# Kernel optimization log

Hardware: AMD Instinct MI355X
Metric: run time of the kernel (lower is better)

## Reference

```python
import jax, jax.numpy as jnp
import numpy as np
from jax import lax

V, D, H, HD, L, E, HID, TOPK, B, T = 32000, 1024, 16, 64, 2, 4, 2048, 2, 1, 1024
EPS = 1e-8


def setup_inputs() -> dict:
    key = jax.random.key(0)
    ks = jax.random.split(key, 10)
    s = 0.02
    so = 0.02 / np.sqrt(2 * L)  # o_proj / down_proj init std
    return dict(
        idx=jax.random.randint(ks[0], (B, T), 0, V),
        tok_emb=jax.random.normal(ks[1], (V, D), jnp.float32) * s,
        attn_norm_w=jnp.ones((L, D), jnp.float32),
        q_w=jax.random.normal(ks[2], (L, D, D), jnp.float32) * s,
        q_b=jnp.zeros((L, D), jnp.float32),
        kv_w=jax.random.normal(ks[3], (L, D, 2 * D), jnp.float32) * s,
        kv_b=jnp.zeros((L, 2 * D), jnp.float32),
        o_w=jax.random.normal(ks[4], (L, D, D), jnp.float32) * so,
        o_b=jnp.zeros((L, D), jnp.float32),
        ffn_norm_w=jnp.ones((L, D), jnp.float32),
        router_w=jax.random.normal(ks[5], (L, D, E), jnp.float32) * s,
        gate_w=jax.random.normal(ks[6], (L, E, D, HID), jnp.float32) * s,
        up_w=jax.random.normal(ks[7], (L, E, D, HID), jnp.float32) * s,
        down_w=jax.random.normal(ks[8], (L, E, HID, D), jnp.float32) * so,
        lnf_w=jnp.ones((D,), jnp.float32),
    )


def _rms(x, w):
    return x / jnp.sqrt(jnp.mean(x * x, axis=-1, keepdims=True) + EPS) * w


def reference(idx, tok_emb, attn_norm_w, q_w, q_b, kv_w, kv_b, o_w, o_b,
              ffn_norm_w, router_w, gate_w, up_w, down_w, lnf_w):
    x = tok_emb[idx]  # [B,T,D]

    # ALiBi bias and causal mask (built once; block_size == T here)
    slopes = jnp.arange(1, H + 1, dtype=jnp.float32) / H          # [H]
    pos = jnp.arange(T, dtype=jnp.float32)
    alibi = slopes[:, None, None] * (pos[None, None, :] - pos[None, :, None])  # [H,T,T]
    causal = jnp.arange(T)[None, :] > jnp.arange(T)[:, None]      # True above diagonal

    for l in range(L):
        # --- causal self-attention with ALiBi ---
        h = _rms(x, attn_norm_w[l])
        q = (h @ q_w[l] + q_b[l]).reshape(B, T, H, HD)
        kv = (h @ kv_w[l] + kv_b[l]).reshape(B, T, 2, H, HD)
        k, v = kv[:, :, 0], kv[:, :, 1]
        att = jnp.einsum('bqhd,bkhd->bhqk', q, k) * (1.0 / np.sqrt(HD))
        att = att + alibi[None]
        att = jnp.where(causal, -jnp.inf, att)
        a = jax.nn.softmax(att, axis=-1)
        y = jnp.einsum('bhqk,bkhd->bqhd', a, v).reshape(B, T, D)
        x = x + y @ o_w[l] + o_b[l]

        # --- MoE FFN (top-k routing, SwiGLU experts, depth-scaled down_proj) ---
        hm = _rms(x, ffn_norm_w[l]).reshape(B * T, D)             # [N,D]
        rlog = hm @ router_w[l]                                   # [N,E]
        vals, sel = lax.top_k(rlog, TOPK)                         # [N,K]
        w = jax.nn.softmax(vals.astype(jnp.float32), axis=-1).astype(hm.dtype)
        # dense per-expert compute, combined sparsely via routing weights
        g = jax.nn.silu(jnp.einsum('nd,edh->enh', hm, gate_w[l])) \
            * jnp.einsum('nd,edh->enh', hm, up_w[l])              # [E,N,HID]
        out_e = jnp.einsum('enh,ehd->end', g, down_w[l]) * (1.0 / np.sqrt(l + 1))
        combine = jnp.sum(jax.nn.one_hot(sel, E, dtype=hm.dtype) * w[..., None], axis=1)  # [N,E]
        moe = jnp.einsum('ne,end->nd', combine, out_e).reshape(B, T, D)
        x = x + moe

    logits = _rms(x, lnf_w) @ tok_emb.T  # tied head weight
    return logits
```

## Files before the change

kernel.cpp:

```cpp
#include <hip/hip_runtime.h>
#include <cmath>

typedef __attribute__((ext_vector_type(8))) _Float16 f16x8;
typedef __attribute__((ext_vector_type(8))) unsigned short u16x8;
typedef __attribute__((ext_vector_type(4))) float f32x4;

#define DEV static __device__ __forceinline__

constexpr int Dm   = 1024;
constexpr int HIDm = 2048;
constexpr int NT   = 1024;
constexpr int NV   = 32000;
constexpr float EPSf  = 1e-8f;
constexpr float LOSC  = 4096.0f;
constexpr float ILOSC = 1.0f / 4096.0f;

DEV unsigned short h2u(_Float16 h){ union{_Float16 h; unsigned short u;} v; v.h=h; return v.u; }

DEV f32x4 MF(f16x8 a, f16x8 b, f32x4 c){ return __builtin_amdgcn_mfma_f32_16x16x32_f16(a,b,c,0,0,0); }

typedef __attribute__((address_space(1))) void GV;
typedef __attribute__((address_space(3))) void LV;
DEV void gll16(const void* g, void* l){
  __builtin_amdgcn_global_load_lds((GV*)(__UINTPTR_TYPE__)g, (LV*)l, 16, 0, 0);
}

DEV int swk(int lane){ return (((lane&3) ^ ((lane>>3)&3))*8); }
DEV int rdc(int fr, int fg){ return ((fg ^ ((fr>>1)&3))*8); }

template<int SPLIT>
DEV void st_sp(unsigned short* __restrict__ hi, unsigned short* __restrict__ lo, size_t o, float v){
  _Float16 hh = (_Float16)v;
  hi[o] = h2u(hh);
  if constexpr (SPLIT==3) lo[o] = h2u((_Float16)((v - (float)hh)*LOSC));
}

__global__ __launch_bounds__(256) void k_gather(
    const int* __restrict__ idx, const float* __restrict__ emb, float* __restrict__ x)
{
  const int t = blockIdx.x;
  const int d = threadIdx.x*4;
  *(float4*)&x[(size_t)t*Dm + d] = *(const float4*)&emb[(size_t)idx[t]*Dm + d];
}

__global__ __launch_bounds__(256) void k_cvt16(
    const float* __restrict__ src, unsigned short* __restrict__ dst)
{
  const size_t i = ((size_t)blockIdx.x*256 + threadIdx.x)*8;
  const float4 v0 = *(const float4*)&src[i];
  const float4 v1 = *(const float4*)&src[i+4];
  u16x8 h;
  h[0]=h2u((_Float16)v0.x); h[1]=h2u((_Float16)v0.y);
  h[2]=h2u((_Float16)v0.z); h[3]=h2u((_Float16)v0.w);
  h[4]=h2u((_Float16)v1.x); h[5]=h2u((_Float16)v1.y);
  h[6]=h2u((_Float16)v1.z); h[7]=h2u((_Float16)v1.w);
  *(u16x8*)&dst[i] = h;
}

template<int SPLIT>
__global__ __launch_bounds__(256) void k_rms(
    const float* __restrict__ x, const float* __restrict__ w,
    unsigned short* __restrict__ ohi, unsigned short* __restrict__ olo)
{
  const int t = blockIdx.x, tid = threadIdx.x;
  const float* row = x + (size_t)t*Dm;
  float s = 0.f;
  #pragma unroll
  for (int i=0;i<4;++i){ const float v = row[tid + i*256]; s += v*v; }
  #pragma unroll
  for (int d=1; d<64; d<<=1) s += __shfl_xor(s, d);
  __shared__ float red[4];
  if ((tid&63)==0) red[tid>>6] = s;
  __syncthreads();
  const float tot = red[0]+red[1]+red[2]+red[3];
  const float rstd = rsqrtf(tot*(1.0f/Dm) + EPSf);
  #pragma unroll
  for (int i=0;i<4;++i){
    const int c = tid + i*256;
    st_sp<SPLIT>(ohi, olo, (size_t)t*Dm + c, row[c]*rstd*w[c]);
  }
}

__global__ __launch_bounds__(64) void k_router(
    const float* __restrict__ x, const float* __restrict__ nw,
    const float* __restrict__ rw, float* __restrict__ cmb)
{
  const int t = blockIdx.x, lane = threadIdx.x;
  const float* row = x + (size_t)t*Dm;
  float ss = 0.f;
  for (int i=lane; i<Dm; i+=64) ss += row[i]*row[i];
  #pragma unroll
  for (int d=1; d<64; d<<=1) ss += __shfl_xor(ss, d);
  const float rstd = rsqrtf(ss*(1.0f/Dm) + EPSf);
  float lg0=0,lg1=0,lg2=0,lg3=0;
  for (int i=lane; i<Dm; i+=64){
    const float hm = row[i]*rstd*nw[i];
    lg0 += hm*rw[i*4+0]; lg1 += hm*rw[i*4+1];
    lg2 += hm*rw[i*4+2]; lg3 += hm*rw[i*4+3];
  }
  #pragma unroll
  for (int d=1; d<64; d<<=1){
    lg0 += __shfl_xor(lg0,d); lg1 += __shfl_xor(lg1,d);
    lg2 += __shfl_xor(lg2,d); lg3 += __shfl_xor(lg3,d);
  }
  if (lane==0){
    float lg[4] = {lg0,lg1,lg2,lg3};
    int s0 = 0;
    for (int e=1;e<4;++e) if (lg[e] > lg[s0]) s0 = e;
    int s1 = -1;
    for (int e=0;e<4;++e){ if (e==s0) continue; if (s1<0 || lg[e] > lg[s1]) s1 = e; }
    const float eb2 = expf(lg[s1] - lg[s0]);
    const float inv = 1.0f/(1.0f + eb2);
    float o[4] = {0.f,0.f,0.f,0.f};
    o[s0] = inv; o[s1] = eb2*inv;
    cmb[t*4+0]=o[0]; cmb[t*4+1]=o[1]; cmb[t*4+2]=o[2]; cmb[t*4+3]=o[3];
  }
}

__global__ __launch_bounds__(256) void k_scan(
    const float* __restrict__ cmb, int* __restrict__ tl,
    float* __restrict__ cwl, int* __restrict__ cnt)
{
  const int e = threadIdx.x>>6, lane = threadIdx.x&63;
  int base = 0;
  for (int t0=0; t0<NT; t0+=64){
    const float w = cmb[(size_t)(t0+lane)*4 + e];
    const unsigned long long m = __ballot(w > 0.f);
    const int pre = __popcll(m & ((1ull<<lane)-1ull));
    if (w > 0.f){ tl[e*NT + base + pre] = t0+lane; cwl[e*NT + base + pre] = w; }
    base += __popcll(m);
  }
  if (lane==0) cnt[e] = base;
}

template<int SPLIT>
__global__ __launch_bounds__(256) void k_wconv(
    const float* __restrict__ W, unsigned short* __restrict__ Whi,
    unsigned short* __restrict__ Wlo, int K, int N)
{
  __shared__ float tile[64][65];
  const int t = threadIdx.x;
  const int n0 = blockIdx.x*64, k0 = blockIdx.y*64;
  const size_t eb = (size_t)blockIdx.z * (size_t)K * N;
  const int r = t>>2;
  #pragma unroll
  for (int i=0;i<4;++i){
    const int c = (t&3)*16 + i*4;
    *(float4*)&tile[r][c] = *(const float4*)&W[eb + (size_t)(k0+r)*N + n0 + c];
  }
  __syncthreads();
  const int n = t>>2;
  #pragma unroll
  for (int i=0;i<2;++i){
    const int kc = (t&3)*8 + i*32;
    u16x8 hi, lo;
    #pragma unroll
    for (int j=0;j<8;++j){
      const float v = tile[kc+j][n];
      const _Float16 hh = (_Float16)v;
      hi[j] = h2u(hh);
      if constexpr (SPLIT==3) lo[j] = h2u((_Float16)((v-(float)hh)*LOSC));
      else lo[j] = 0;
    }
    *(u16x8*)&Whi[eb + (size_t)(n0+n)*K + k0 + kc] = hi;
    if constexpr (SPLIT==3) *(u16x8*)&Wlo[eb + (size_t)(n0+n)*K + k0 + kc] = lo;
  }
}

template<int SPLIT, int ZMODE>
__global__ __launch_bounds__(256) void k_mm(
    const unsigned short* __restrict__ Ahi, const unsigned short* __restrict__ Alo,
    const unsigned short* __restrict__ Bhi, const unsigned short* __restrict__ Blo,
    float* __restrict__ part, int lda, int ldb, int K, int ldo)
{
  constexpr int PL = (SPLIT==3)?2:1;
  __shared__ __align__(16) unsigned short As[PL][128][32];
  __shared__ __align__(16) unsigned short Bs[PL][128][32];
  const int tid=threadIdx.x, wv=tid>>6, lane=tid&63, fr=lane&15, fg=lane>>4;
  const int n0=blockIdx.x*128, r0=blockIdx.y*128, zz=blockIdx.z;
  const int wr=(wv>>1)*64, wc=(wv&1)*64;
  const int sr=lane>>2, sk=swk(lane);
  const int rc = rdc(fr, fg);

  const f32x4 z4={0.f,0.f,0.f,0.f};
  f32x4 accM[4][4], accC[4][4];
  #pragma unroll
  for (int i=0;i<4;++i)
    #pragma unroll
    for (int j=0;j<4;++j){ accM[i][j]=z4; accC[i][j]=z4; }

  for (int kt=0; kt<K; kt+=32){
    #pragma unroll
    for (int i=0;i<2;++i){
      const int rr = wv*32 + i*16 + sr;
      size_t ao, bo;
      if constexpr (ZMODE==2){
        ao = (size_t)(r0+rr)*lda + zz*K + kt + sk;
        bo = (size_t)(n0+rr)*ldb + zz*K + kt + sk;
      } else {
// ... 13 lines not shown
      for (int p=0;p<PL;++p) a[rt][p] = *(const f16x8*)&As[p][wr+rt*16+fr][rc];
    #pragma unroll
    for (int ct=0;ct<4;++ct)
      #pragma unroll
      for (int p=0;p<PL;++p) b[ct][p] = *(const f16x8*)&Bs[p][wc+ct*16+fr][rc];
    #pragma unroll
    for (int rt=0;rt<4;++rt)
      #pragma unroll
      for (int ct=0;ct<4;++ct){
        accM[rt][ct] = MF(a[rt][0], b[ct][0], accM[rt][ct]);
        if constexpr (SPLIT==3){
          accC[rt][ct] = MF(a[rt][0], b[ct][1], accC[rt][ct]);
          accC[rt][ct] = MF(a[rt][1], b[ct][0], accC[rt][ct]);
        }
      }
    __syncthreads();
  }

  #pragma unroll
  for (int rt=0;rt<4;++rt)
    #pragma unroll
    for (int ct=0;ct<4;++ct)
      #pragma unroll
      for (int j=0;j<4;++j){
        const int row = r0 + wr + rt*16 + fg*4 + j;
        const int col = n0 + wc + ct*16 + fr;
        float v = accM[rt][ct][j];
        if constexpr (SPLIT==3) v += accC[rt][ct][j]*ILOSC;
        part[((size_t)zz*NT + row)*ldo + col] = v;
      }
}

template<int SPLIT>
__global__ __launch_bounds__(256) void k_comb_qk(
    const float* __restrict__ part, const float* __restrict__ qb, const float* __restrict__ kvb,
    unsigned short* __restrict__ qhi, unsigned short* __restrict__ qlo,
    unsigned short* __restrict__ khi, unsigned short* __restrict__ klo)
{
  const int t = blockIdx.x;
  #pragma unroll
  for (int i=0;i<2;++i){
    const int col = threadIdx.x*4 + i*1024;
    const float4 p0 = *(const float4*)&part[(size_t)t*3072 + col];
    const float4 p1 = *(const float4*)&part[((size_t)NT + t)*3072 + col];
    float v[4] = {p0.x+p1.x, p0.y+p1.y, p0.z+p1.z, p0.w+p1.w};
    #pragma unroll
    for (int j=0;j<4;++j){
      const int c = col + j;
      if (c < Dm) st_sp<SPLIT>(qhi, qlo, (size_t)t*Dm + c, v[j] + qb[c]);
      else        st_sp<SPLIT>(khi, klo, (size_t)t*Dm + (c-Dm), v[j] + kvb[c-Dm]);
    }
  }
}

template<int SPLIT>
__global__ __launch_bounds__(256) void k_combvT(
    const float* __restrict__ part, const float* __restrict__ kvb,
    unsigned short* __restrict__ vthi, unsigned short* __restrict__ vtlo)
{
  __shared__ float tile[64][65];
  const int d0 = blockIdx.x*64, t0 = blockIdx.y*64;
  const int tid = threadIdx.x;
  {
    const int tl_ = tid>>2, dc = (tid&3)*16;
    #pragma unroll
    for (int i=0;i<4;++i){
      const int d = dc + i*4;
      const float4 p0 = *(const float4*)&part[(size_t)(t0+tl_)*3072 + 2048 + d0 + d];
      const float4 p1 = *(const float4*)&part[((size_t)NT + t0+tl_)*3072 + 2048 + d0 + d];
      tile[tl_][d+0] = p0.x+p1.x + kvb[1024+d0+d+0];
      tile[tl_][d+1] = p0.y+p1.y + kvb[1024+d0+d+1];
      tile[tl_][d+2] = p0.z+p1.z + kvb[1024+d0+d+2];
      tile[tl_][d+3] = p0.w+p1.w + kvb[1024+d0+d+3];
    }
  }
  __syncthreads();
  #pragma unroll
  for (int i=0;i<2;++i){
    const int u = tid + i*256;
    const int dl = u>>3, tch = (u&7)*8;
    u16x8 hi, lo;
    #pragma unroll
    for (int j=0;j<8;++j){
      const float v = tile[tch+j][dl];
      const _Float16 hh = (_Float16)v;
      hi[j] = h2u(hh);
      if constexpr (SPLIT==3) lo[j] = h2u((_Float16)((v-(float)hh)*LOSC));
      else lo[j] = 0;
    }
    *(u16x8*)&vthi[(size_t)(d0+dl)*NT + t0 + tch] = hi;
    if constexpr (SPLIT==3) *(u16x8*)&vtlo[(size_t)(d0+dl)*NT + t0 + tch] = lo;
  }
}

template<int SPLIT>
__global__ __launch_bounds__(256) void k_down(
    const unsigned short* __restrict__ Ahi, const unsigned short* __restrict__ Alo,
    const unsigned short* __restrict__ Bhi, const unsigned short* __restrict__ Blo,
    const int* __restrict__ tl, const int* __restrict__ cnt,
    float* __restrict__ part)
{
  constexpr int PL = (SPLIT==3)?2:1;
  const int zz = blockIdx.z, e = zz>>1, ks = zz&1;
  const int r0 = blockIdx.y*128, n0 = blockIdx.x*128;
  const int cn = cnt[e];
  if (r0 >= cn) return;
  __shared__ __align__(16) unsigned short As[PL][128][32];
  __shared__ __align__(16) unsigned short Bs[PL][128][32];
  __shared__ int tl_s[128];
  const int tid=threadIdx.x, wv=tid>>6, lane=tid&63, fr=lane&15, fg=lane>>4;
  const int wr=(wv>>1)*64, wc=(wv&1)*64;
  const int sr=lane>>2, sk=swk(lane);
  const int rc = rdc(fr, fg);
  if (tid < 128) tl_s[tid] = (r0+tid < cn) ? tl[e*NT + r0 + tid] : -1;

  const f32x4 z4={0.f,0.f,0.f,0.f};
  f32x4 accM[4][4], accC[4][4];
  #pragma unroll
  for (int i=0;i<4;++i)
    #pragma unroll
    for (int j=0;j<4;++j){ accM[i][j]=z4; accC[i][j]=z4; }

  const int kbeg = ks*1024, kend = kbeg + 1024;
  for (int kt=kbeg; kt<kend; kt+=32){
// ... 13 lines not shown
    for (int rt=0;rt<4;++rt)
      #pragma unroll
      for (int p=0;p<PL;++p) a[rt][p] = *(const f16x8*)&As[p][wr+rt*16+fr][rc];
    #pragma unroll
    for (int ct=0;ct<4;++ct)
      #pragma unroll
      for (int p=0;p<PL;++p) b[ct][p] = *(const f16x8*)&Bs[p][wc+ct*16+fr][rc];
    #pragma unroll
    for (int rt=0;rt<4;++rt)
      #pragma unroll
      for (int ct=0;ct<4;++ct){
        accM[rt][ct] = MF(a[rt][0], b[ct][0], accM[rt][ct]);
        if constexpr (SPLIT==3){
          accC[rt][ct] = MF(a[rt][0], b[ct][1], accC[rt][ct]);
          accC[rt][ct] = MF(a[rt][1], b[ct][0], accC[rt][ct]);
        }
      }
    __syncthreads();
  }

  #pragma unroll
  for (int rt=0;rt<4;++rt)
    #pragma unroll
    for (int ct=0;ct<4;++ct)
      #pragma unroll
      for (int j=0;j<4;++j){
        const int i = wr + rt*16 + fg*4 + j;
        const int col = n0 + wc + ct*16 + fr;
        float v = accM[rt][ct][j];
        if constexpr (SPLIT==3) v += accC[rt][ct][j]*ILOSC;
        const int tok = tl_s[i];
        if (tok >= 0) part[((size_t)zz*NT + tok)*Dm + col] = v;
      }
}

template<int SK, bool BIAS>
__global__ __launch_bounds__(256) void k_comb(
    const float* __restrict__ part, const float* __restrict__ bias, float* __restrict__ x)
{
  const int row = blockIdx.x;
  const int c = threadIdx.x*4;
  float4 s = *(float4*)&x[(size_t)row*Dm + c];
  #pragma unroll
  for (int z=0; z<SK; ++z){
    const float4 p = *(const float4*)&part[((size_t)z*NT + row)*Dm + c];
    s.x+=p.x; s.y+=p.y; s.z+=p.z; s.w+=p.w;
  }
  if constexpr (BIAS){
    const float4 b = *(const float4*)&bias[c];
    s.x+=b.x; s.y+=b.y; s.z+=b.z; s.w+=b.w;
  }
  *(float4*)&x[(size_t)row*Dm + c] = s;
}

__global__ __launch_bounds__(256) void k_comb_moe(
    const float* __restrict__ part, const float* __restrict__ cmb, float* __restrict__ x)
{
  const int row = blockIdx.x;
  const int c = threadIdx.x*4;
  float4 s = *(float4*)&x[(size_t)row*Dm + c];
  #pragma unroll
  for (int e=0; e<4; ++e){
    if (cmb[(size_t)row*4 + e] > 0.f){
      const float4 p0 = *(const float4*)&part[((size_t)(e*2+0)*NT + row)*Dm + c];
      const float4 p1 = *(const float4*)&part[((size_t)(e*2+1)*NT + row)*Dm + c];
      s.x+=p0.x+p1.x; s.y+=p0.y+p1.y; s.z+=p0.z+p1.z; s.w+=p0.w+p1.w;
    }
  }
  *(float4*)&x[(size_t)row*Dm + c] = s;
}

template<int SPLIT>
__global__ __launch_bounds__(512) void k_guf(
    const unsigned short* __restrict__ Ahi, const unsigned short* __restrict__ Alo,
    const unsigned short* __restrict__ Ghi, const unsigned short* __restrict__ Glo,
    const unsigned short* __restrict__ Uhi, const unsigned short* __restrict__ Ulo,
    const int* __restrict__ tl, const float* __restrict__ cwl, const int* __restrict__ cnt,
    unsigned short* __restrict__ Hhi, unsigned short* __restrict__ Hlo, float scale)
{
  constexpr int PL=(SPLIT==3)?2:1;
  const int e = blockIdx.z, r0 = blockIdx.y*128, n0 = blockIdx.x*64;
  const int cn = cnt[e];
  if (r0 >= cn) return;
  __shared__ __align__(16) unsigned short As[PL][128][32];
  __shared__ __align__(16) unsigned short Gs[PL][64][32];
  __shared__ __align__(16) unsigned short Us[PL][64][32];
  __shared__ float cw_s[128];
  const int tid=threadIdx.x, wv=tid>>6, lane=tid&63, fr=lane&15, fg=lane>>4;
  const int wr=(wv>>1)*32, wc=(wv&1)*32;
  const int sr=lane>>2, sk=swk(lane);
  const int rc = rdc(fr, fg);
  const size_t ebW = (size_t)e * ((size_t)HIDm*Dm);
  if (tid < 128) cw_s[tid] = (r0+tid < cn) ? cwl[e*NT + r0 + tid]*scale : 0.f;

  const int lrA = r0 + wv*16 + sr;
  const int tokA = tl[e*NT + (lrA < cn ? lrA : cn-1)];
  const size_t abase = (size_t)tokA*Dm + sk;
  const int rrB = (wv&3)*16 + sr;
  const size_t bbase = ebW + (size_t)(n0+rrB)*Dm + sk;

  const f32x4 z4={0.f,0.f,0.f,0.f};
  f32x4 aGM[2][2],aGC[2][2],aUM[2][2],aUC[2][2];
// ... 99 lines not shown
      h1[2]=h2u((_Float16)v2.z); h1[3]=h2u((_Float16)v2.w);
      h1[4]=h2u((_Float16)v3.x); h1[5]=h2u((_Float16)v3.y);
      h1[6]=h2u((_Float16)v3.z); h1[7]=h2u((_Float16)v3.w);
      const int s_ = (br>>1)&3;
      const int u0 = (tid&1)*2;
      *(u16x8*)&Bs[br][(u0^s_)*8]     = h0;
      *(u16x8*)&Bs[br][((u0+1)^s_)*8] = h1;
    }
    __syncthreads();
    f16x8 a[4], b[4];
    #pragma unroll
    for (int rt=0;rt<4;++rt) a[rt] = *(const f16x8*)&As[wr+rt*16+fr][rc];
    #pragma unroll
    for (int ct=0;ct<4;++ct) b[ct] = *(const f16x8*)&Bs[wc+ct*16+fr][rc];
    #pragma unroll
    for (int rt=0;rt<4;++rt)
      #pragma unroll
      for (int ct=0;ct<4;++ct) acc[rt][ct] = MF(a[rt], b[ct], acc[rt][ct]);
    __syncthreads();
  }
  #pragma unroll
  for (int rt=0;rt<4;++rt)
    #pragma unroll
    for (int ct=0;ct<4;++ct)
      #pragma unroll
      for (int j=0;j<4;++j)
        out[(size_t)(r0+wr+rt*16+fg*4+j)*NV + n0+wc+ct*16+fr] = acc[rt][ct][j];
}

__global__ __launch_bounds__(256) void k_lg16(
    const unsigned short* __restrict__ Ahi, const unsigned short* __restrict__ B16,
    float* __restrict__ out)
{
  __shared__ __align__(16) unsigned short As[128][32];
  __shared__ __align__(16) unsigned short Bs[128][32];
  const int tid=threadIdx.x, wv=tid>>6, lane=tid&63, fr=lane&15, fg=lane>>4;
  const int w = (blockIdx.x & 7)*250 + (blockIdx.x >> 3);
  const int n0 = (w>>3)*128, r0 = (w&7)*128;
  const int wr=(wv>>1)*64, wc=(wv&1)*64;
  const int sr=lane>>2, sk=swk(lane);
  const int rc = rdc(fr, fg);
  const f32x4 z4={0.f,0.f,0.f,0.f};
  f32x4 acc[4][4];
  #pragma unroll
  for (int i=0;i<4;++i)
    #pragma unroll
    for (int j=0;j<4;++j) acc[i][j]=z4;

  for (int kt=0; kt<Dm; kt+=32){
    #pragma unroll
    for (int i=0;i<2;++i){
      const int rr = wv*32 + i*16 + sr;
      gll16(&Ahi[(size_t)(r0+rr)*Dm + kt + sk], &As[wv*32+i*16][0]);
      gll16(&B16[(size_t)(n0+rr)*Dm + kt + sk], &Bs[wv*32+i*16][0]);
    }
    __syncthreads();
    f16x8 a[4], b[4];
    #pragma unroll
    for (int rt=0;rt<4;++rt) a[rt] = *(const f16x8*)&As[wr+rt*16+fr][rc];
    #pragma unroll
    for (int ct=0;ct<4;++ct) b[ct] = *(const f16x8*)&Bs[wc+ct*16+fr][rc];
    #pragma unroll
    for (int rt=0;rt<4;++rt)
      #pragma unroll
      for (int ct=0;ct<4;++ct) acc[rt][ct] = MF(a[rt], b[ct], acc[rt][ct]);
    __syncthreads();
  }
  #pragma unroll
  for (int rt=0;rt<4;++rt)
    #pragma unroll
    for (int ct=0;ct<4;++ct)
      #pragma unroll
      for (int j=0;j<4;++j)
        out[(size_t)(r0+wr+rt*16+fg*4+j)*NV + n0+wc+ct*16+fr] = acc[rt][ct][j];
}

template<int SPLIT>
__global__ __launch_bounds__(256) void k_attn(
    const unsigned short* __restrict__ qhi, const unsigned short* __restrict__ qlo,
    const unsigned short* __restrict__ khi, const unsigned short* __restrict__ klo,
    const unsigned short* __restrict__ vthi, const unsigned short* __restrict__ vtlo,
    unsigned short* __restrict__ yhi, unsigned short* __restrict__ ylo)
{
  constexpr int PL = (SPLIT==3) ? 2 : 1;
  const int qt = blockIdx.x, hd = blockIdx.y;
  const int tid = threadIdx.x, wv = tid>>6, lane = tid&63;
  const int fr = lane&15, fg = lane>>4;
  const int rbase = qt*64 + wv*16;
  const float slope = (float)(hd+1) * (1.0f/16.0f);

  __shared__ __align__(16) unsigned short Ps[4][PL][16][32];

  f16x8 aq[2][PL];
  #pragma unroll
  for (int c=0;c<2;++c){
    const size_t off = (size_t)(rbase+fr)*Dm + hd*64 + c*32 + fg*8;
    aq[c][0] = *(const f16x8*)&qhi[off];
    if constexpr (SPLIT==3) aq[c][1] = *(const f16x8*)&qlo[off];
// ... 90 lines not shown
      const size_t off = (size_t)(hd*64 + ct*16 + fr)*NT + kt*32 + fg*8;
      const f16x8 v0 = *(const f16x8*)&vthi[off];
      yM[ct] = MF(pa[0], v0, yM[ct]);
      if constexpr (SPLIT==3){
        const f16x8 v1 = *(const f16x8*)&vtlo[off];
        yC[ct] = MF(pa[0], v1, yC[ct]);
        yC[ct] = MF(pa[1], v0, yC[ct]);
      }
    }
    asm volatile("s_waitcnt lgkmcnt(0)" ::: "memory");
  }
  #pragma unroll
  for (int ct=0;ct<4;++ct)
    #pragma unroll
    for (int j=0;j<4;++j){
      float v = yM[ct][j];
      if constexpr (SPLIT==3) v += yC[ct][j]*ILOSC;
      v /= lsum[j];
      const size_t off = (size_t)(rbase + fg*4 + j)*Dm + hd*64 + ct*16 + fr;
      st_sp<SPLIT>(yhi, ylo, off, v);
    }
}

struct Ptrs {
  float* x; float* cmb; float* part; float* cwl; int* tl; int* cnt;
  unsigned short *hhi,*hlo,*qhi,*qlo,*khi,*klo,*vthi,*vtlo,*yhi,*ylo,*Hhi,*Hlo;
  unsigned short *Wqkvh,*Wqkvl,*WOh,*WOl,*WGh,*WGl,*WUh,*WUl,*WDh,*WDl;
};

template<int S>
static void run_layer(const Ptrs& P, int l,
    const float* anw, const float* qw, const float* qb, const float* kvw, const float* kvb,
    const float* ow, const float* ob, const float* fnw, const float* rw,
    const float* gw, const float* uw, const float* dw, float scale, hipStream_t stream)
{
  k_rms<S><<<dim3(NT), dim3(256), 0, stream>>>(P.x, anw + l*Dm, P.hhi, P.hlo);
  k_wconv<S><<<dim3(16,16,1), dim3(256), 0, stream>>>(qw + (size_t)l*Dm*Dm, P.Wqkvh, P.Wqkvl, Dm, Dm);
  k_wconv<S><<<dim3(32,16,1), dim3(256), 0, stream>>>(kvw + (size_t)l*Dm*2*Dm,
      P.Wqkvh + (size_t)Dm*Dm, P.Wqkvl + (size_t)Dm*Dm, Dm, 2*Dm);
  k_wconv<S><<<dim3(16,16,1), dim3(256), 0, stream>>>(ow + (size_t)l*Dm*Dm, P.WOh, P.WOl, Dm, Dm);
  k_mm<S,2><<<dim3(24,8,2), dim3(256), 0, stream>>>(P.hhi, P.hlo, P.Wqkvh, P.Wqkvl,
      P.part, Dm, Dm, 512, 3072);
  k_comb_qk<S><<<dim3(NT), dim3(256), 0, stream>>>(P.part, qb + l*Dm, kvb + l*2*Dm,
      P.qhi, P.qlo, P.khi, P.klo);
  k_combvT<S><<<dim3(16,16), dim3(256), 0, stream>>>(P.part, kvb + l*2*Dm, P.vthi, P.vtlo);
  k_attn<S><<<dim3(16,16), dim3(256), 0, stream>>>(P.qhi,P.qlo,P.khi,P.klo,P.vthi,P.vtlo,P.yhi,P.ylo);
  k_mm<S,2><<<dim3(8,8,4), dim3(256), 0, stream>>>(P.yhi, P.ylo, P.WOh, P.WOl,
      P.part, Dm, Dm, 256, Dm);
  k_comb<4,true><<<dim3(NT), dim3(256), 0, stream>>>(P.part, ob + l*Dm, P.x);
  k_router<<<dim3(NT), dim3(64), 0, stream>>>(P.x, fnw + l*Dm, rw + (size_t)l*Dm*4, P.cmb);
  k_scan<<<dim3(1), dim3(256), 0, stream>>>(P.cmb, P.tl, P.cwl, P.cnt);
  k_rms<S><<<dim3(NT), dim3(256), 0, stream>>>(P.x, fnw + l*Dm, P.hhi, P.hlo);
  k_wconv<S><<<dim3(32,16,4), dim3(256), 0, stream>>>(gw + (size_t)l*4*Dm*HIDm, P.WGh, P.WGl, Dm, HIDm);
  k_wconv<S><<<dim3(32,16,4), dim3(256), 0, stream>>>(uw + (size_t)l*4*Dm*HIDm, P.WUh, P.WUl, Dm, HIDm);
  k_guf<S><<<dim3(32,8,4), dim3(512), 0, stream>>>(P.hhi, P.hlo, P.WGh, P.WGl, P.WUh, P.WUl,
      P.tl, P.cwl, P.cnt, P.Hhi, P.Hlo, scale);
  k_wconv<S><<<dim3(16,32,4), dim3(256), 0, stream>>>(dw + (size_t)l*4*HIDm*Dm, P.WDh, P.WDl, HIDm, Dm);
  k_down<S><<<dim3(8,8,8), dim3(256), 0, stream>>>(P.Hhi, P.Hlo, P.WDh, P.WDl,
      P.tl, P.cnt, P.part);
  k_comb_moe<<<dim3(NT), dim3(256), 0, stream>>>(P.part, P.cmb, P.x);
}

extern "C" void kernel_launch(void* const* d_in, const int* in_sizes, int n_in,
                              void* d_out, int out_size, void* d_ws, size_t ws_size,
                              hipStream_t stream)
{
  (void)in_sizes; (void)n_in; (void)out_size;
  const int*   idx = (const int*)d_in[0];
  const float* emb = (const float*)d_in[1];
  const float* anw = (const float*)d_in[2];
  const float* qw  = (const float*)d_in[3];
  const float* qb  = (const float*)d_in[4];
  const float* kvw = (const float*)d_in[5];
  const float* kvb = (const float*)d_in[6];
  const float* ow  = (const float*)d_in[7];
  const float* ob  = (const float*)d_in[8];
  const float* fnw = (const float*)d_in[9];
  const float* rw  = (const float*)d_in[10];
  const float* gw  = (const float*)d_in[11];
  const float* uw  = (const float*)d_in[12];
  const float* dw  = (const float*)d_in[13];
  const float* lnf = (const float*)d_in[14];

  constexpr size_t MB = (size_t)1<<20;
  constexpr size_t KB = (size_t)1<<10;
  char* sc = (char*)d_out;
  Ptrs P;
  P.x     = (float*)sc;
  P.hhi   = (unsigned short*)(sc + 4*MB);
  P.hlo   = (unsigned short*)(sc + 6*MB);
  P.qhi   = (unsigned short*)(sc + 8*MB);
  P.qlo   = (unsigned short*)(sc + 10*MB);
  P.khi   = (unsigned short*)(sc + 12*MB);
  P.klo   = (unsigned short*)(sc + 14*MB);
  P.vthi  = (unsigned short*)(sc + 16*MB);
  P.vtlo  = (unsigned short*)(sc + 18*MB);
  P.yhi   = (unsigned short*)(sc + 20*MB);
  P.ylo   = (unsigned short*)(sc + 22*MB);
  P.cmb   = (float*)(sc + 24*MB);
  P.tl    = (int*)(sc + 24*MB + 64*KB);
  P.cwl   = (float*)(sc + 24*MB + 128*KB);
  P.cnt   = (int*)(sc + 24*MB + 192*KB);
  P.Hhi   = (unsigned short*)(sc + 25*MB);
  P.Hlo   = (unsigned short*)(sc + 41*MB);
  P.Wqkvh = (unsigned short*)(sc + 57*MB);
  P.Wqkvl = (unsigned short*)(sc + 63*MB);
  P.WOh   = (unsigned short*)(sc + 69*MB);
  P.WOl   = (unsigned short*)(sc + 71*MB);
  P.WGh   = (unsigned short*)(sc + 57*MB);
  P.WGl   = (unsigned short*)(sc + 73*MB);
  P.WUh   = (unsigned short*)(sc + 89*MB);
  P.WUl   = (unsigned short*)(sc + 105*MB);
  P.WDh   = (unsigned short*)(sc + 57*MB);
  P.WDl   = (unsigned short*)(sc + 73*MB);
  P.part  = (float*)(sc + 89*MB);
  unsigned short* xhat  = (unsigned short*)d_ws;
  unsigned short* emb16 = (unsigned short*)((char*)d_ws + 2*MB);
  const bool big_ws = ws_size >= 68*MB;
  float* out = (float*)d_out;

  if (big_ws)
    k_cvt16<<<dim3(NV*Dm/(256*8)), dim3(256), 0, stream>>>(emb, emb16);
  k_gather<<<dim3(NT), dim3(256), 0, stream>>>(idx, emb, P.x);

  run_layer<3>(P, 0, anw, qw, qb, kvw, kvb, ow, ob, fnw, rw, gw, uw, dw, 1.0f, stream);
  run_layer<1>(P, 1, anw, qw, qb, kvw, kvb, ow, ob, fnw, rw, gw, uw, dw, 0.70710678f, stream);

  k_rms<1><<<dim3(NT), dim3(256), 0, stream>>>(P.x, lnf, xhat, nullptr);
  if (big_ws)
    k_lg16<<<dim3(2000), dim3(256), 0, stream>>>(xhat, emb16, out);
  else
    k_lg<<<dim3(2000), dim3(256), 0, stream>>>(xhat, emb, out);
}
```

Before: 860.6 us.

## Fuse residual/norm/router kernels, batch weight conversions, and widen logits K-tile

Merges the gather and embedding fp16 conversion into one launch. Folds the o-proj residual add, RMSNorm and router into a single kernel, and the MoE combine into the next layer's norm or the final norm. Batches the q/kv/o and gate/up weight conversions into single launches and merges the q/k and transposed-v combine kernels. The logits matmul now uses a 64-wide K tile with a new swizzle, two MFMAs per stage. This cuts launch count and re-reads of x, at the cost of more LDS in the logits kernel.

```diff
diff --git a/kernel.cpp b/kernel.cpp
--- a/kernel.cpp
+++ b/kernel.cpp
@@ -35,26 +35,26 @@
   if constexpr (SPLIT==3) lo[o] = h2u((_Float16)((v - (float)hh)*LOSC));
 }
 
-__global__ __launch_bounds__(256) void k_gather(
-    const int* __restrict__ idx, const float* __restrict__ emb, float* __restrict__ x)
-{
-  const int t = blockIdx.x;
-  const int d = threadIdx.x*4;
-  *(float4*)&x[(size_t)t*Dm + d] = *(const float4*)&emb[(size_t)idx[t]*Dm + d];
-}
-
-__global__ __launch_bounds__(256) void k_cvt16(
-    const float* __restrict__ src, unsigned short* __restrict__ dst)
-{
-  const size_t i = ((size_t)blockIdx.x*256 + threadIdx.x)*8;
-  const float4 v0 = *(const float4*)&src[i];
-  const float4 v1 = *(const float4*)&src[i+4];
-  u16x8 h;
-  h[0]=h2u((_Float16)v0.x); h[1]=h2u((_Float16)v0.y);
-  h[2]=h2u((_Float16)v0.z); h[3]=h2u((_Float16)v0.w);
-  h[4]=h2u((_Float16)v1.x); h[5]=h2u((_Float16)v1.y);
-  h[6]=h2u((_Float16)v1.z); h[7]=h2u((_Float16)v1.w);
-  *(u16x8*)&dst[i] = h;
+__global__ __launch_bounds__(256) void k_init(
+    const int* __restrict__ idx, const float* __restrict__ emb,
+    float* __restrict__ x, unsigned short* __restrict__ emb16, int gbase)
+{
+  const int b = blockIdx.x;
+  if (b < gbase){
+    const size_t i = ((size_t)b*256 + threadIdx.x)*8;
+    const float4 v0 = *(const float4*)&emb[i];
+    const float4 v1 = *(const float4*)&emb[i+4];
+    u16x8 h;
+    h[0]=h2u((_Float16)v0.x); h[1]=h2u((_Float16)v0.y);
+    h[2]=h2u((_Float16)v0.z); h[3]=h2u((_Float16)v0.w);
+    h[4]=h2u((_Float16)v1.x); h[5]=h2u((_Float16)v1.y);
+    h[6]=h2u((_Float16)v1.z); h[7]=h2u((_Float16)v1.w);
+    *(u16x8*)&emb16[i] = h;
+  } else {
+    const int t = b - gbase;
+    const int d = threadIdx.x*4;
+    *(float4*)&x[(size_t)t*Dm + d] = *(const float4*)&emb[(size_t)idx[t]*Dm + d];
+  }
 }
 
 template<int SPLIT>
@@ -81,40 +81,99 @@
   }
 }
 
-__global__ __launch_bounds__(64) void k_router(
-    const float* __restrict__ x, const float* __restrict__ nw,
-    const float* __restrict__ rw, float* __restrict__ cmb)
-{
-  const int t = blockIdx.x, lane = threadIdx.x;
-  const float* row = x + (size_t)t*Dm;
-  float ss = 0.f;
-  for (int i=lane; i<Dm; i+=64) ss += row[i]*row[i];
+template<int SPLIT>
+__global__ __launch_bounds__(256) void k_fuse_o(
+    const float* __restrict__ part, const float* __restrict__ ob,
+    const float* __restrict__ fnw, const float* __restrict__ rw,
+    float* __restrict__ x, unsigned short* __restrict__ hhi,
+    unsigned short* __restrict__ hlo, float* __restrict__ cmb)
+{
+  const int t = blockIdx.x, tid = threadIdx.x, wv = tid>>6, lane = tid&63;
+  const int c = tid*4;
+  float4 s = *(float4*)&x[(size_t)t*Dm + c];
+  #pragma unroll
+  for (int z=0; z<4; ++z){
+    const float4 p = *(const float4*)&part[((size_t)z*NT + t)*Dm + c];
+    s.x+=p.x; s.y+=p.y; s.z+=p.z; s.w+=p.w;
+  }
+  const float4 b4 = *(const float4*)&ob[c];
+  s.x+=b4.x; s.y+=b4.y; s.z+=b4.z; s.w+=b4.w;
+  *(float4*)&x[(size_t)t*Dm + c] = s;
+
+  float ss = s.x*s.x + s.y*s.y + s.z*s.z + s.w*s.w;
   #pragma unroll
   for (int d=1; d<64; d<<=1) ss += __shfl_xor(ss, d);
-  const float rstd = rsqrtf(ss*(1.0f/Dm) + EPSf);
-  float lg0=0,lg1=0,lg2=0,lg3=0;
-  for (int i=lane; i<Dm; i+=64){
-    const float hm = row[i]*rstd*nw[i];
-    lg0 += hm*rw[i*4+0]; lg1 += hm*rw[i*4+1];
-    lg2 += hm*rw[i*4+2]; lg3 += hm*rw[i*4+3];
+  __shared__ float red[4];
+  if (lane==0) red[wv] = ss;
+  __syncthreads();
+  const float rstd = rsqrtf((red[0]+red[1]+red[2]+red[3])*(1.0f/Dm) + EPSf);
+
+  const float4 w4 = *(const float4*)&fnw[c];
+  const float sv[4] = {s.x,s.y,s.z,s.w};
+  const float wv4[4] = {w4.x,w4.y,w4.z,w4.w};
+  float hm[4];
+  float lg[4] = {0.f,0.f,0.f,0.f};
+  #pragma unroll
+  for (int j=0;j<4;++j){
+    hm[j] = sv[j]*rstd*wv4[j];
+    st_sp<SPLIT>(hhi, hlo, (size_t)t*Dm + c + j, hm[j]);
+    const float4 r4 = *(const float4*)&rw[(size_t)(c+j)*4];
+    lg[0] += hm[j]*r4.x; lg[1] += hm[j]*r4.y; lg[2] += hm[j]*r4.z; lg[3] += hm[j]*r4.w;
   }
   #pragma unroll
   for (int d=1; d<64; d<<=1){
-    lg0 += __shfl_xor(lg0,d); lg1 += __shfl_xor(lg1,d);
-    lg2 += __shfl_xor(lg2,d); lg3 += __shfl_xor(lg3,d);
-  }
-  if (lane==0){
-    float lg[4] = {lg0,lg1,lg2,lg3};
+    lg[0]+=__shfl_xor(lg[0],d); lg[1]+=__shfl_xor(lg[1],d);
+    lg[2]+=__shfl_xor(lg[2],d); lg[3]+=__shfl_xor(lg[3],d);
+  }
+  __shared__ float red2[4][4];
+  if (lane==0){ red2[wv][0]=lg[0]; red2[wv][1]=lg[1]; red2[wv][2]=lg[2]; red2[wv][3]=lg[3]; }
+  __syncthreads();
+  if (tid==0){
+    float L[4];
+    #pragma unroll
+    for (int e=0;e<4;++e) L[e] = red2[0][e]+red2[1][e]+red2[2][e]+red2[3][e];
     int s0 = 0;
-    for (int e=1;e<4;++e) if (lg[e] > lg[s0]) s0 = e;
+    for (int e=1;e<4;++e) if (L[e] > L[s0]) s0 = e;
     int s1 = -1;
-    for (int e=0;e<4;++e){ if (e==s0) continue; if (s1<0 || lg[e] > lg[s1]) s1 = e; }
-    const float eb2 = expf(lg[s1] - lg[s0]);
+    for (int e=0;e<4;++e){ if (e==s0) continue; if (s1<0 || L[e] > L[s1]) s1 = e; }
+    const float eb2 = expf(L[s1] - L[s0]);
     const float inv = 1.0f/(1.0f + eb2);
     float o[4] = {0.f,0.f,0.f,0.f};
     o[s0] = inv; o[s1] = eb2*inv;
     cmb[t*4+0]=o[0]; cmb[t*4+1]=o[1]; cmb[t*4+2]=o[2]; cmb[t*4+3]=o[3];
   }
+}
+
+__global__ __launch_bounds__(256) void k_fuse_moe(
+    const float* __restrict__ part, const float* __restrict__ cmb,
+    const float* __restrict__ w, float* __restrict__ x,
+    unsigned short* __restrict__ dst, int writex)
+{
+  const int t = blockIdx.x, tid = threadIdx.x, wv = tid>>6, lane = tid&63;
+  const int c = tid*4;
+  float4 s = *(float4*)&x[(size_t)t*Dm + c];
+  #pragma unroll
+  for (int e=0; e<4; ++e){
+    if (cmb[(size_t)t*4 + e] > 0.f){
+      const float4 p0 = *(const float4*)&part[((size_t)(e*2+0)*NT + t)*Dm + c];
+      const float4 p1 = *(const float4*)&part[((size_t)(e*2+1)*NT + t)*Dm + c];
+      s.x+=p0.x+p1.x; s.y+=p0.y+p1.y; s.z+=p0.z+p1.z; s.w+=p0.w+p1.w;
+    }
+  }
+  if (writex) *(float4*)&x[(size_t)t*Dm + c] = s;
+  float ss = s.x*s.x + s.y*s.y + s.z*s.z + s.w*s.w;
+  #pragma unroll
+  for (int d=1; d<64; d<<=1) ss += __shfl_xor(ss, d);
+  __shared__ float red[4];
+  if (lane==0) red[wv] = ss;
+  __syncthreads();
+  const float rstd = rsqrtf((red[0]+red[1]+red[2]+red[3])*(1.0f/Dm) + EPSf);
+  const float4 w4 = *(const float4*)&w[c];
+  const float sv[4] = {s.x,s.y,s.z,s.w};
+  const float wv4[4] = {w4.x,w4.y,w4.z,w4.w};
+  #pragma unroll
+  for (int j=0;j<4;++j)
+    dst[(size_t)t*Dm + c + j] = h2u((_Float16)(sv[j]*rstd*wv4[j]));
 }
 
 __global__ __launch_bounds__(256) void k_scan(
@@ -134,19 +193,15 @@
 }
 
 template<int SPLIT>
-__global__ __launch_bounds__(256) void k_wconv(
-    const float* __restrict__ W, unsigned short* __restrict__ Whi,
-    unsigned short* __restrict__ Wlo, int K, int N)
-{
-  __shared__ float tile[64][65];
-  const int t = threadIdx.x;
-  const int n0 = blockIdx.x*64, k0 = blockIdx.y*64;
-  const size_t eb = (size_t)blockIdx.z * (size_t)K * N;
+DEV void wconv_tile(const float* __restrict__ W, unsigned short* __restrict__ Whi,
+                    unsigned short* __restrict__ Wlo, int K, int N, int n0, int k0,
+                    float (*tile)[65], int t)
+{
   const int r = t>>2;
   #pragma unroll
   for (int i=0;i<4;++i){
     const int c = (t&3)*16 + i*4;
-    *(float4*)&tile[r][c] = *(const float4*)&W[eb + (size_t)(k0+r)*N + n0 + c];
+    *(float4*)&tile[r][c] = *(const float4*)&W[(size_t)(k0+r)*N + n0 + c];
   }
   __syncthreads();
   const int n = t>>2;
@@ -162,9 +217,59 @@
       if constexpr (SPLIT==3) lo[j] = h2u((_Float16)((v-(float)hh)*LOSC));
       else lo[j] = 0;
     }
-    *(u16x8*)&Whi[eb + (size_t)(n0+n)*K + k0 + kc] = hi;
-    if constexpr (SPLIT==3) *(u16x8*)&Wlo[eb + (size_t)(n0+n)*K + k0 + kc] = lo;
-  }
+    *(u16x8*)&Whi[(size_t)(n0+n)*K + k0 + kc] = hi;
+    if constexpr (SPLIT==3) *(u16x8*)&Wlo[(size_t)(n0+n)*K + k0 + kc] = lo;
+  }
+}
+
+template<int SPLIT>
+__global__ __launch_bounds__(256) void k_wconv(
+    const float* __restrict__ W, unsigned short* __restrict__ Whi,
+    unsigned short* __restrict__ Wlo, int K, int N)
+{
+  __shared__ float tile[64][65];
+  const size_t eb = (size_t)blockIdx.z * (size_t)K * N;
+  wconv_tile<SPLIT>(W + eb, Whi + eb, Wlo + eb, K, N, blockIdx.x*64, blockIdx.y*64,
+                    tile, threadIdx.x);
+}
+
+template<int SPLIT>
+__global__ __launch_bounds__(256) void k_wconv_qkvo(
+    const float* __restrict__ qw, const float* __restrict__ kvw, const float* __restrict__ ow,
+    unsigned short* __restrict__ Wh, unsigned short* __restrict__ Wl,
+    unsigned short* __restrict__ WOh, unsigned short* __restrict__ WOl)
+{
+  __shared__ float tile[64][65];
+  const int b = blockIdx.x, t = threadIdx.x;
+  if (b < 256){
+    wconv_tile<SPLIT>(qw, Wh, Wl, Dm, Dm, (b&15)*64, (b>>4)*64, tile, t);
+  } else if (b < 768){
+    const int c = b - 256;
+    wconv_tile<SPLIT>(kvw, Wh + (size_t)Dm*Dm, Wl + (size_t)Dm*Dm,
+                      Dm, 2*Dm, (c&31)*64, (c>>5)*64, tile, t);
+  } else {
+    const int c = b - 768;
+    wconv_tile<SPLIT>(ow, WOh, WOl, Dm, Dm, (c&15)*64, (c>>4)*64, tile, t);
+  }
+}
+
+template<int SPLIT>
+__global__ __launch_bounds__(256) void k_wconv_gu(
+    const float* __restrict__ gw, const float* __restrict__ uw,
+    unsigned short* __restrict__ WGh, unsigned short* __restrict__ WGl,
+    unsigned short* __restrict__ WUh, unsigned short* __restrict__ WUl)
+{
+  __shared__ float tile[64][65];
+  const int b = blockIdx.x, t = threadIdx.x;
+  const int half = b >> 11;
+  const int c = b & 2047;
+  const int e = c >> 9, cc = c & 511;
+  const size_t eb = (size_t)e * (size_t)Dm * HIDm;
+  const int n0 = (cc&31)*64, k0 = (cc>>5)*64;
+  if (half == 0)
+    wconv_tile<SPLIT>(gw + eb, WGh + eb, WGl + eb, Dm, HIDm, n0, k0, tile, t);
+  else
+    wconv_tile<SPLIT>(uw + eb, WUh + eb, WUl + eb, Dm, HIDm, n0, k0, tile, t);
 }
 
 template<int SPLIT, int ZMODE>
@@ -244,64 +349,62 @@
 }
 
 template<int SPLIT>
-__global__ __launch_bounds__(256) void k_comb_qk(
+__global__ __launch_bounds__(256) void k_comb_qkvt(
     const float* __restrict__ part, const float* __restrict__ qb, const float* __restrict__ kvb,
     unsigned short* __restrict__ qhi, unsigned short* __restrict__ qlo,
-    unsigned short* __restrict__ khi, unsigned short* __restrict__ klo)
-{
-  const int t = blockIdx.x;
-  #pragma unroll
-  for (int i=0;i<2;++i){
-    const int col = threadIdx.x*4 + i*1024;
-    const float4 p0 = *(const float4*)&part[(size_t)t*3072 + col];
-    const float4 p1 = *(const float4*)&part[((size_t)NT + t)*3072 + col];
-    float v[4] = {p0.x+p1.x, p0.y+p1.y, p0.z+p1.z, p0.w+p1.w};
-    #pragma unroll
-    for (int j=0;j<4;++j){
-      const int c = col + j;
-      if (c < Dm) st_sp<SPLIT>(qhi, qlo, (size_t)t*Dm + c, v[j] + qb[c]);
-      else        st_sp<SPLIT>(khi, klo, (size_t)t*Dm + (c-Dm), v[j] + kvb[c-Dm]);
-    }
-  }
-}
-
-template<int SPLIT>
-__global__ __launch_bounds__(256) void k_combvT(
-    const float* __restrict__ part, const float* __restrict__ kvb,
+    unsigned short* __restrict__ khi, unsigned short* __restrict__ klo,
     unsigned short* __restrict__ vthi, unsigned short* __restrict__ vtlo)
 {
   __shared__ float tile[64][65];
-  const int d0 = blockIdx.x*64, t0 = blockIdx.y*64;
-  const int tid = threadIdx.x;
-  {
-    const int tl_ = tid>>2, dc = (tid&3)*16;
-    #pragma unroll
-    for (int i=0;i<4;++i){
-      const int d = dc + i*4;
-      const float4 p0 = *(const float4*)&part[(size_t)(t0+tl_)*3072 + 2048 + d0 + d];
-      const float4 p1 = *(const float4*)&part[((size_t)NT + t0+tl_)*3072 + 2048 + d0 + d];
-      tile[tl_][d+0] = p0.x+p1.x + kvb[1024+d0+d+0];
-      tile[tl_][d+1] = p0.y+p1.y + kvb[1024+d0+d+1];
-      tile[tl_][d+2] = p0.z+p1.z + kvb[1024+d0+d+2];
-      tile[tl_][d+3] = p0.w+p1.w + kvb[1024+d0+d+3];
-    }
-  }
-  __syncthreads();
-  #pragma unroll
-  for (int i=0;i<2;++i){
-    const int u = tid + i*256;
-    const int dl = u>>3, tch = (u&7)*8;
-    u16x8 hi, lo;
-    #pragma unroll
-    for (int j=0;j<8;++j){
-      const float v = tile[tch+j][dl];
-      const _Float16 hh = (_Float16)v;
-      hi[j] = h2u(hh);
-      if constexpr (SPLIT==3) lo[j] = h2u((_Float16)((v-(float)hh)*LOSC));
-      else lo[j] = 0;
-    }
-    *(u16x8*)&vthi[(size_t)(d0+dl)*NT + t0 + tch] = hi;
-    if constexpr (SPLIT==3) *(u16x8*)&vtlo[(size_t)(d0+dl)*NT + t0 + tch] = lo;
+  const int bid = blockIdx.x, tid = threadIdx.x;
+  if (bid < 1024){
+    const int t = bid;
+    #pragma unroll
+    for (int i=0;i<2;++i){
+      const int col = tid*4 + i*1024;
+      const float4 p0 = *(const float4*)&part[(size_t)t*3072 + col];
+      const float4 p1 = *(const float4*)&part[((size_t)NT + t)*3072 + col];
+      float v[4] = {p0.x+p1.x, p0.y+p1.y, p0.z+p1.z, p0.w+p1.w};
+      #pragma unroll
+      for (int j=0;j<4;++j){
+        const int c = col + j;
+        if (c < Dm) st_sp<SPLIT>(qhi, qlo, (size_t)t*Dm + c, v[j] + qb[c]);
+        else        st_sp<SPLIT>(khi, klo, (size_t)t*Dm + (c-Dm), v[j] + kvb[c-Dm]);
+      }
+    }
+  } else {
+    const int c = bid - 1024;
+    const int d0 = (c&15)*64, t0 = (c>>4)*64;
+    {
+      const int tl_ = tid>>2, dc = (tid&3)*16;
+      #pragma unroll
+      for (int i=0;i<4;++i){
+        const int d = dc + i*4;
+        const float4 p0 = *(const float4*)&part[(size_t)(t0+tl_)*3072 + 2048 + d0 + d];
+        const float4 p1 = *(const float4*)&part[((size_t)NT + t0+tl_)*3072 + 2048 + d0 + d];
+        tile[tl_][d+0] = p0.x+p1.x + kvb[1024+d0+d+0];
+        tile[tl_][d+1] = p0.y+p1.y + kvb[1024+d0+d+1];
+        tile[tl_][d+2] = p0.z+p1.z + kvb[1024+d0+d+2];
+        tile[tl_][d+3] = p0.w+p1.w + kvb[1024+d0+d+3];
+      }
+    }
+    __syncthreads();
+    #pragma unroll
+    for (int i=0;i<2;++i){
+      const int u = tid + i*256;
+      const int dl = u>>3, tch = (u&7)*8;
+      u16x8 hi, lo;
+      #pragma unroll
+      for (int j=0;j<8;++j){
+        const float v = tile[tch+j][dl];
+        const _Float16 hh = (_Float16)v;
+        hi[j] = h2u(hh);
+        if constexpr (SPLIT==3) lo[j] = h2u((_Float16)((v-(float)hh)*LOSC));
+        else lo[j] = 0;
+      }
+      *(u16x8*)&vthi[(size_t)(d0+dl)*NT + t0 + tch] = hi;
+      if constexpr (SPLIT==3) *(u16x8*)&vtlo[(size_t)(d0+dl)*NT + t0 + tch] = lo;
+    }
   }
 }
 
@@ -381,42 +484,6 @@
         const int tok = tl_s[i];
         if (tok >= 0) part[((size_t)zz*NT + tok)*Dm + col] = v;
       }
-}
-
-template<int SK, bool BIAS>
-__global__ __launch_bounds__(256) void k_comb(
-    const float* __restrict__ part, const float* __restrict__ bias, float* __restrict__ x)
-{
-  const int row = blockIdx.x;
-  const int c = threadIdx.x*4;
-  float4 s = *(float4*)&x[(size_t)row*Dm + c];
-  #pragma unroll
-  for (int z=0; z<SK; ++z){
-    const float4 p = *(const float4*)&part[((size_t)z*NT + row)*Dm + c];
-    s.x+=p.x; s.y+=p.y; s.z+=p.z; s.w+=p.w;
-  }
-  if constexpr (BIAS){
-    const float4 b = *(const float4*)&bias[c];
-    s.x+=b.x; s.y+=b.y; s.z+=b.z; s.w+=b.w;
-  }
-  *(float4*)&x[(size_t)row*Dm + c] = s;
-}
-
-__global__ __launch_bounds__(256) void k_comb_moe(
-    const float* __restrict__ part, const float* __restrict__ cmb, float* __restrict__ x)
-{
-  const int row = blockIdx.x;
-  const int c = threadIdx.x*4;
-  float4 s = *(float4*)&x[(size_t)row*Dm + c];
-  #pragma unroll
-  for (int e=0; e<4; ++e){
-    if (cmb[(size_t)row*4 + e] > 0.f){
-      const float4 p0 = *(const float4*)&part[((size_t)(e*2+0)*NT + row)*Dm + c];
-      const float4 p1 = *(const float4*)&part[((size_t)(e*2+1)*NT + row)*Dm + c];
-      s.x+=p0.x+p1.x; s.y+=p0.y+p1.y; s.z+=p0.z+p1.z; s.w+=p0.w+p1.w;
-    }
-  }
-  *(float4*)&x[(size_t)row*Dm + c] = s;
 }
 
 template<int SPLIT>
@@ -582,14 +649,14 @@
     const unsigned short* __restrict__ Ahi, const unsigned short* __restrict__ B16,
     float* __restrict__ out)
 {
-  __shared__ __align__(16) unsigned short As[128][32];
-  __shared__ __align__(16) unsigned short Bs[128][32];
+  __shared__ __align__(16) unsigned short As[128][64];
+  __shared__ __align__(16) unsigned short Bs[128][64];
   const int tid=threadIdx.x, wv=tid>>6, lane=tid&63, fr=lane&15, fg=lane>>4;
   const int w = (blockIdx.x & 7)*250 + (blockIdx.x >> 3);
   const int n0 = (w>>3)*128, r0 = (w&7)*128;
   const int wr=(wv>>1)*64, wc=(wv&1)*64;
-  const int sr=lane>>2, sk=swk(lane);
-  const int rc = rdc(fr, fg);
+  const int srow = lane>>3;
+  const int sk = (((lane&7) ^ srow)*8);
   const f32x4 z4={0.f,0.f,0.f,0.f};
   f32x4 acc[4][4];
   #pragma unroll
@@ -597,23 +664,32 @@
     #pragma unroll
     for (int j=0;j<4;++j) acc[i][j]=z4;
 
-  for (int kt=0; kt<Dm; kt+=32){
-    #pragma unroll
-    for (int i=0;i<2;++i){
-      const int rr = wv*32 + i*16 + sr;
-      gll16(&Ahi[(size_t)(r0+rr)*Dm + kt + sk], &As[wv*32+i*16][0]);
-      gll16(&B16[(size_t)(n0+rr)*Dm + kt + sk], &Bs[wv*32+i*16][0]);
-    }
-    __syncthreads();
-    f16x8 a[4], b[4];
-    #pragma unroll
-    for (int rt=0;rt<4;++rt) a[rt] = *(const f16x8*)&As[wr+rt*16+fr][rc];
-    #pragma unroll
-    for (int ct=0;ct<4;++ct) b[ct] = *(const f16x8*)&Bs[wc+ct*16+fr][rc];
+  for (int kt=0; kt<Dm; kt+=64){
+    #pragma unroll
+    for (int i=0;i<4;++i){
+      const int rr = wv*32 + i*8 + srow;
+      gll16(&Ahi[(size_t)(r0+rr)*Dm + kt + sk], &As[wv*32+i*8][0]);
+      gll16(&B16[(size_t)(n0+rr)*Dm + kt + sk], &Bs[wv*32+i*8][0]);
+    }
+    __syncthreads();
+    f16x8 a[4][2], b[4][2];
     #pragma unroll
     for (int rt=0;rt<4;++rt)
       #pragma unroll
-      for (int ct=0;ct<4;++ct) acc[rt][ct] = MF(a[rt], b[ct], acc[rt][ct]);
+      for (int kk=0;kk<2;++kk)
+        a[rt][kk] = *(const f16x8*)&As[wr+rt*16+fr][(((kk*4+fg) ^ (fr&7))*8)];
+    #pragma unroll
+    for (int ct=0;ct<4;++ct)
+      #pragma unroll
+      for (int kk=0;kk<2;++kk)
+        b[ct][kk] = *(const f16x8*)&Bs[wc+ct*16+fr][(((kk*4+fg) ^ (fr&7))*8)];
+    #pragma unroll
+    for (int rt=0;rt<4;++rt)
+      #pragma unroll
+      for (int ct=0;ct<4;++ct){
+        acc[rt][ct] = MF(a[rt][0], b[ct][0], acc[rt][ct]);
+        acc[rt][ct] = MF(a[rt][1], b[ct][1], acc[rt][ct]);
+      }
     __syncthreads();
   }
   #pragma unroll
@@ -770,33 +846,31 @@
 static void run_layer(const Ptrs& P, int l,
     const float* anw, const float* qw, const float* qb, const float* kvw, const float* kvb,
     const float* ow, const float* ob, const float* fnw, const float* rw,
-    const float* gw, const float* uw, const float* dw, float scale, hipStream_t stream)
-{
-  k_rms<S><<<dim3(NT), dim3(256), 0, stream>>>(P.x, anw + l*Dm, P.hhi, P.hlo);
-  k_wconv<S><<<dim3(16,16,1), dim3(256), 0, stream>>>(qw + (size_t)l*Dm*Dm, P.Wqkvh, P.Wqkvl, Dm, Dm);
-  k_wconv<S><<<dim3(32,16,1), dim3(256), 0, stream>>>(kvw + (size_t)l*Dm*2*Dm,
-      P.Wqkvh + (size_t)Dm*Dm, P.Wqkvl + (size_t)Dm*Dm, Dm, 2*Dm);
-  k_wconv<S><<<dim3(16,16,1), dim3(256), 0, stream>>>(ow + (size_t)l*Dm*Dm, P.WOh, P.WOl, Dm, Dm);
+    const float* gw, const float* uw, const float* dw,
+    const float* nextw, unsigned short* nextdst, int writex, float scale, hipStream_t stream)
+{
+  (void)anw;
+  k_wconv_qkvo<S><<<dim3(1024), dim3(256), 0, stream>>>(
+      qw + (size_t)l*Dm*Dm, kvw + (size_t)l*Dm*2*Dm, ow + (size_t)l*Dm*Dm,
+      P.Wqkvh, P.Wqkvl, P.WOh, P.WOl);
   k_mm<S,2><<<dim3(24,8,2), dim3(256), 0, stream>>>(P.hhi, P.hlo, P.Wqkvh, P.Wqkvl,
       P.part, Dm, Dm, 512, 3072);
-  k_comb_qk<S><<<dim3(NT), dim3(256), 0, stream>>>(P.part, qb + l*Dm, kvb + l*2*Dm,
-      P.qhi, P.qlo, P.khi, P.klo);
-  k_combvT<S><<<dim3(16,16), dim3(256), 0, stream>>>(P.part, kvb + l*2*Dm, P.vthi, P.vtlo);
+  k_comb_qkvt<S><<<dim3(1280), dim3(256), 0, stream>>>(P.part, qb + l*Dm, kvb + l*2*Dm,
+      P.qhi, P.qlo, P.khi, P.klo, P.vthi, P.vtlo);
   k_attn<S><<<dim3(16,16), dim3(256), 0, stream>>>(P.qhi,P.qlo,P.khi,P.klo,P.vthi,P.vtlo,P.yhi,P.ylo);
   k_mm<S,2><<<dim3(8,8,4), dim3(256), 0, stream>>>(P.yhi, P.ylo, P.WOh, P.WOl,
       P.part, Dm, Dm, 256, Dm);
-  k_comb<4,true><<<dim3(NT), dim3(256), 0, stream>>>(P.part, ob + l*Dm, P.x);
-  k_router<<<dim3(NT), dim3(64), 0, stream>>>(P.x, fnw + l*Dm, rw + (size_t)l*Dm*4, P.cmb);
+  k_fuse_o<S><<<dim3(NT), dim3(256), 0, stream>>>(P.part, ob + l*Dm, fnw + l*Dm,
+      rw + (size_t)l*Dm*4, P.x, P.hhi, P.hlo, P.cmb);
   k_scan<<<dim3(1), dim3(256), 0, stream>>>(P.cmb, P.tl, P.cwl, P.cnt);
-  k_rms<S><<<dim3(NT), dim3(256), 0, stream>>>(P.x, fnw + l*Dm, P.hhi, P.hlo);
-  k_wconv<S><<<dim3(32,16,4), dim3(256), 0, stream>>>(gw + (size_t)l*4*Dm*HIDm, P.WGh, P.WGl, Dm, HIDm);
-  k_wconv<S><<<dim3(32,16,4), dim3(256), 0, stream>>>(uw + (size_t)l*4*Dm*HIDm, P.WUh, P.WUl, Dm, HIDm);
+  k_wconv_gu<S><<<dim3(4096), dim3(256), 0, stream>>>(
+      gw + (size_t)l*4*Dm*HIDm, uw + (size_t)l*4*Dm*HIDm, P.WGh, P.WGl, P.WUh, P.WUl);
   k_guf<S><<<dim3(32,8,4), dim3(512), 0, stream>>>(P.hhi, P.hlo, P.WGh, P.WGl, P.WUh, P.WUl,
       P.tl, P.cwl, P.cnt, P.Hhi, P.Hlo, scale);
   k_wconv<S><<<dim3(16,32,4), dim3(256), 0, stream>>>(dw + (size_t)l*4*HIDm*Dm, P.WDh, P.WDl, HIDm, Dm);
   k_down<S><<<dim3(8,8,8), dim3(256), 0, stream>>>(P.Hhi, P.Hlo, P.WDh, P.WDl,
       P.tl, P.cnt, P.part);
-  k_comb_moe<<<dim3(NT), dim3(256), 0, stream>>>(P.part, P.cmb, P.x);
+  k_fuse_moe<<<dim3(NT), dim3(256), 0, stream>>>(P.part, P.cmb, nextw, P.x, nextdst, writex);
 }
 
 extern "C" void kernel_launch(void* const* d_in, const int* in_sizes, int n_in,
@@ -857,14 +931,15 @@
   const bool big_ws = ws_size >= 68*MB;
   float* out = (float*)d_out;
 
-  if (big_ws)
-    k_cvt16<<<dim3(NV*Dm/(256*8)), dim3(256), 0, stream>>>(emb, emb16);
-  k_gather<<<dim3(NT), dim3(256), 0, stream>>>(idx, emb, P.x);
-
-  run_layer<3>(P, 0, anw, qw, qb, kvw, kvb, ow, ob, fnw, rw, gw, uw, dw, 1.0f, stream);
-  run_layer<1>(P, 1, anw, qw, qb, kvw, kvb, ow, ob, fnw, rw, gw, uw, dw, 0.70710678f, stream);
-
-  k_rms<1><<<dim3(NT), dim3(256), 0, stream>>>(P.x, lnf, xhat, nullptr);
+  const int gbase = big_ws ? 16000 : 0;
+  k_init<<<dim3(gbase + NT), dim3(256), 0, stream>>>(idx, emb, P.x, emb16, gbase);
+  k_rms<3><<<dim3(NT), dim3(256), 0, stream>>>(P.x, anw, P.hhi, P.hlo);
+
+  run_layer<3>(P, 0, anw, qw, qb, kvw, kvb, ow, ob, fnw, rw, gw, uw, dw,
+               anw + Dm, P.hhi, 1, 1.0f, stream);
+  run_layer<1>(P, 1, anw, qw, qb, kvw, kvb, ow, ob, fnw, rw, gw, uw, dw,
+               lnf, xhat, 0, 0.70710678f, stream);
+
   if (big_ws)
     k_lg16<<<dim3(2000), dim3(256), 0, stream>>>(xhat, emb16, out);
   else
```

After: 794.9 us. 1.08x faster.
